# Kernel tuning notes

Measured on AMD Instinct MI355X. Metric: run time of the kernel, lower is better.

Reference implementation:

```python
import jax, jax.numpy as jnp
import numpy as np

SIZE = 4096


def fast_hadamard_transform(x, normalize=True):
    """Walsh-Hadamard transform along last dim via log2(n) butterfly stages."""
    orig_shape = x.shape
    n = orig_shape[-1]
    h = 1
    while h < n:
        # view as (..., n//(2h), 2, h) and butterfly the pair axis
        x = x.reshape(orig_shape[:-1] + (n // (2 * h), 2, h))
        a = x[..., 0, :]
        b = x[..., 1, :]
        x = jnp.stack([a + b, a - b], axis=-2).reshape(orig_shape)
        h *= 2
    if normalize:
        x = x * (1.0 / np.sqrt(n)).astype(x.dtype)
    return x


def setup_inputs() -> dict:
    key = jax.random.key(0)
    kx, ks, kb = jax.random.split(key, 3)
    x = jax.random.normal(kx, (4, 4096, SIZE), dtype=jnp.float32)
    # adaptive_init: scale ~ N(1.0, 0.1), shift ~ N(0.0, 0.01)
    scale = 1.0 + 0.1 * jax.random.normal(ks, (SIZE,), dtype=jnp.float32)
    shift = 0.01 * jax.random.normal(kb, (SIZE,), dtype=jnp.float32)
    return {"x": x, "scale": scale, "shift": shift}


def reference(x, scale, shift):
    x_h = fast_hadamard_transform(x, normalize=True)
    return scale * x_h + shift
```

## Files before the change

kernel.cpp:

```cpp
#include <hip/hip_runtime.h>


#define ROW 4096
#define STR 17

__device__ __forceinline__ void wht16(float v[16]) {
#pragma unroll
  for (int h = 1; h < 16; h <<= 1) {
#pragma unroll
    for (int i = 0; i < 16; ++i) {
      if ((i & h) == 0) {
        float a = v[i], b = v[i | h];
        v[i] = a + b;
        v[i | h] = a - b;
      }
    }
  }
}

__global__ __launch_bounds__(256) void AdaptiveHadamardTransform_kernel(
    const float* __restrict__ x, const float* __restrict__ scale,
    const float* __restrict__ shift, float* __restrict__ out) {
  __shared__ float lds[256 * STR];

  const int t = threadIdx.x;
  const long long base = (long long)blockIdx.x * ROW;

  float v[16];

  const float4* __restrict__ x4 = reinterpret_cast<const float4*>(x + base + 16 * t);
#pragma unroll
  for (int j = 0; j < 4; ++j) {
    const float4 f = x4[j];
    v[4 * j + 0] = f.x;
    v[4 * j + 1] = f.y;
    v[4 * j + 2] = f.z;
    v[4 * j + 3] = f.w;
  }
  wht16(v);

#pragma unroll
  for (int j = 0; j < 16; ++j) lds[t * STR + j] = v[j];
  __syncthreads();

  {
    const int i2 = t >> 4, i0 = t & 15;
#pragma unroll
    for (int r = 0; r < 16; ++r) v[r] = lds[(i2 * 16 + r) * STR + i0];
    wht16(v);
#pragma unroll
    for (int r = 0; r < 16; ++r) lds[(i2 * 16 + r) * STR + i0] = v[r];
  }
  __syncthreads();

  {
    const int i1 = t >> 4, i0 = t & 15;
#pragma unroll
    for (int r = 0; r < 16; ++r) v[r] = lds[(r * 16 + i1) * STR + i0];
  }
  wht16(v);

  const float norm = 0.015625f;
#pragma unroll
  for (int r = 0; r < 16; ++r) {
    const int c = r * 256 + t;
    const float o = fmaf(scale[c], v[r] * norm, shift[c]);
    __builtin_nontemporal_store(o, out + base + c);
  }
}

extern "C" void kernel_launch(void* const* d_in, const int* in_sizes, int n_in,
                              void* d_out, int out_size, void* d_ws, size_t ws_size,
                              hipStream_t stream) {
  const float* x = (const float*)d_in[0];
  const float* scale = (const float*)d_in[1];
  const float* shift = (const float*)d_in[2];
  float* out = (float*)d_out;

  const int rows = in_sizes[0] / ROW;
  AdaptiveHadamardTransform_kernel<<<rows, 256, 0, stream>>>(x, scale, shift, out);
}
```

Measured before the change: 441.3 us.

## Replace middle LDS WHT stage with ds_swizzle butterflies across lanes

```diff
diff --git a/kernel.cpp b/kernel.cpp
--- a/kernel.cpp
+++ b/kernel.cpp
@@ -3,6 +3,8 @@
 
 #define ROW 4096
 #define STR 17
+
+typedef int intx1;
 
 __device__ __forceinline__ void wht16(float v[16]) {
 #pragma unroll
@@ -18,46 +20,55 @@
   }
 }
 
-__global__ __launch_bounds__(256) void AdaptiveHadamardTransform_kernel(
+template <int PAT>
+__device__ __forceinline__ void swz_step(float v[16], float sgn) {
+#pragma unroll
+  for (int j = 0; j < 16; ++j) {
+    const int pi = __builtin_amdgcn_ds_swizzle(__float_as_int(v[j]), PAT);
+    v[j] = fmaf(sgn, v[j], __int_as_float(pi));
+  }
+}
+
+__global__ __launch_bounds__(256, 8) void AdaptiveHadamardTransform_kernel(
     const float* __restrict__ x, const float* __restrict__ scale,
     const float* __restrict__ shift, float* __restrict__ out) {
   __shared__ float lds[256 * STR];
 
   const int t = threadIdx.x;
+  const int lane = t & 63;
   const long long base = (long long)blockIdx.x * ROW;
 
   float v[16];
 
-  const float4* __restrict__ x4 = reinterpret_cast<const float4*>(x + base + 16 * t);
+  {
+    const float4* __restrict__ x4 =
+        reinterpret_cast<const float4*>(x + base + 16 * t);
 #pragma unroll
-  for (int j = 0; j < 4; ++j) {
-    const float4 f = x4[j];
-    v[4 * j + 0] = f.x;
-    v[4 * j + 1] = f.y;
-    v[4 * j + 2] = f.z;
-    v[4 * j + 3] = f.w;
+    for (int q = 0; q < 4; ++q) {
+      const float4 f = x4[q];
+      v[4 * q + 0] = f.x;
+      v[4 * q + 1] = f.y;
+      v[4 * q + 2] = f.z;
+      v[4 * q + 3] = f.w;
+    }
   }
+
   wht16(v);
+
+  swz_step<0x041F>(v, (lane & 1) ? -1.f : 1.f);
+  swz_step<0x081F>(v, (lane & 2) ? -1.f : 1.f);
+  swz_step<0x101F>(v, (lane & 4) ? -1.f : 1.f);
+  swz_step<0x201F>(v, (lane & 8) ? -1.f : 1.f);
 
 #pragma unroll
   for (int j = 0; j < 16; ++j) lds[t * STR + j] = v[j];
   __syncthreads();
-
-  {
-    const int i2 = t >> 4, i0 = t & 15;
-#pragma unroll
-    for (int r = 0; r < 16; ++r) v[r] = lds[(i2 * 16 + r) * STR + i0];
-    wht16(v);
-#pragma unroll
-    for (int r = 0; r < 16; ++r) lds[(i2 * 16 + r) * STR + i0] = v[r];
-  }
-  __syncthreads();
-
   {
     const int i1 = t >> 4, i0 = t & 15;
 #pragma unroll
     for (int r = 0; r < 16; ++r) v[r] = lds[(r * 16 + i1) * STR + i0];
   }
+
   wht16(v);
 
   const float norm = 0.015625f;
```

New measurement: 437.2 us. About the same (-0.9%).
